# Kernel tuning notes

Hardware: AMD Instinct MI355X
Metric: run time of the kernel (lower is better)

The kernel has to match this reference:

```python
import jax, jax.numpy as jnp
import numpy as np

D = 768
H = 8
HD = D // H
FF = 4 * D


def _linear_params(key, din, dout):
    kw, kb = jax.random.split(key)
    lim = 1.0 / np.sqrt(din)
    W = jax.random.uniform(kw, (din, dout), jnp.float32, -lim, lim)
    b = jax.random.uniform(kb, (dout,), jnp.float32, -lim, lim)
    return W, b


def setup_inputs() -> dict:
    key = jax.random.key(0)
    ks = jax.random.split(key, 8)
    x = jax.random.normal(ks[0], (16, 1024, D), jnp.float32)
    Wq, bq = _linear_params(ks[1], D, D)
    Wk, bk = _linear_params(ks[2], D, D)
    Wv, bv = _linear_params(ks[3], D, D)
    Wo, bo = _linear_params(ks[4], D, D)
    W1, b1 = _linear_params(ks[5], D, FF)
    W2, b2 = _linear_params(ks[6], FF, D)
    gamma = jnp.ones((D,), jnp.float32)
    beta = jnp.zeros((D,), jnp.float32)
    return {"x": x, "gamma": gamma, "beta": beta,
            "Wq": Wq, "bq": bq, "Wk": Wk, "bk": bk, "Wv": Wv, "bv": bv,
            "Wo": Wo, "bo": bo, "W1": W1, "b1": b1, "W2": W2, "b2": b2}


def _layernorm(x, gamma, beta, eps=1e-5):
    mu = jnp.mean(x, axis=-1, keepdims=True)
    var = jnp.var(x, axis=-1, keepdims=True)
    return (x - mu) * jax.lax.rsqrt(var + eps) * gamma + beta


def _block(x, gamma, beta, Wq, bq, Wk, bk, Wv, bv, Wo, bo, W1, b1, W2, b2):
    b, n, d = x.shape
    residual = x
    h = _layernorm(x, gamma, beta)
    # QKV projections -> [b, h, n, hd]
    q = (h @ Wq + bq).reshape(b, n, H, HD).transpose(0, 2, 1, 3)
    k = (h @ Wk + bk).reshape(b, n, H, HD).transpose(0, 2, 1, 3)
    v = (h @ Wv + bv).reshape(b, n, H, HD).transpose(0, 2, 1, 3)
    scale = HD ** 0.5
    scores = jnp.einsum('bhid,bhjd->bhij', q, k) / scale
    attn = jax.nn.softmax(scores, axis=-1)
    out = jnp.einsum('bhij,bhjd->bhid', attn, v)
    out = out.transpose(0, 2, 1, 3).reshape(b, n, d)
    out = out @ Wo + bo
    out = out + residual
    residual = out
    h = _layernorm(out, gamma, beta)  # same LN params reused (as in source)
    h = jax.nn.gelu(h @ W1 + b1, approximate=False)
    h = h @ W2 + b2
    return h + residual


def reference(x, gamma, beta, Wq, bq, Wk, bk, Wv, bv, Wo, bo, W1, b1, W2, b2):
    return _block(x, gamma, beta, Wq, bq, Wk, bk, Wv, bv, Wo, bo, W1, b1, W2, b2)
```

## Files before the change

### kernel.cpp

```cpp
#include <hip/hip_runtime.h>

typedef unsigned short u16;
typedef float f32x4 __attribute__((ext_vector_type(4)));
typedef __bf16 bf16x8 __attribute__((ext_vector_type(8)));

#define AS1 __attribute__((address_space(1)))
#define AS3 __attribute__((address_space(3)))

__device__ __forceinline__ float bf2f(u16 h) {
  return __uint_as_float(((unsigned)h) << 16);
}
__device__ __forceinline__ u16 f2bf(float f) {
  unsigned u = __float_as_uint(f);
  unsigned r = (u + 0x7FFFu + ((u >> 16) & 1u)) >> 16;
  return (u16)r;
}
__device__ __forceinline__ void gload16(const u16* g, u16* l) {
  __builtin_amdgcn_global_load_lds((const AS1 void*)g, (AS3 void*)l, 16, 0, 0);
}

__global__ void transpose_k(const float* __restrict__ in, u16* __restrict__ out,
                            int R, int C) {
  __shared__ u16 t[32][33];
  int c0 = blockIdx.x * 32, r0 = blockIdx.y * 32;
  int tx = threadIdx.x & 31, ty = threadIdx.x >> 5;
  for (int i = 0; i < 32; i += 8)
    t[ty + i][tx] = f2bf(in[(size_t)(r0 + ty + i) * C + c0 + tx]);
  __syncthreads();
  for (int i = 0; i < 32; i += 8)
    out[(size_t)(c0 + ty + i) * R + r0 + tx] = t[tx][ty + i];
}

__global__ void vtrans_k(const u16* __restrict__ v, u16* __restrict__ vt) {
  __shared__ u16 t[32][33];
  int bh = blockIdx.z, b = bh >> 3, h = bh & 7;
  int n0 = blockIdx.y * 32, d0 = blockIdx.x * 32;
  int tx = threadIdx.x & 31, ty = threadIdx.x >> 5;
  const u16* src = v + (size_t)(b * 1024) * 768 + h * 96;
  for (int i = 0; i < 32; i += 8)
    t[ty + i][tx] = src[(size_t)(n0 + ty + i) * 768 + d0 + tx];
  __syncthreads();
  u16* dst = vt + ((size_t)bh * 96 + d0) * 1024 + n0;
  for (int i = 0; i < 32; i += 8)
    dst[(size_t)(ty + i) * 1024 + tx] = t[tx][ty + i];
}

__global__ __launch_bounds__(256) void ln_f32_k(const float* __restrict__ x,
                                                const float* __restrict__ gamma,
                                                const float* __restrict__ beta,
                                                u16* __restrict__ out) {
  __shared__ float red[8];
  int row = blockIdx.x, t = threadIdx.x;
  const float* xr = x + (size_t)row * 768;
  float v[3], s = 0.f, s2 = 0.f;
#pragma unroll
  for (int i = 0; i < 3; i++) {
    v[i] = xr[t + i * 256];
    s += v[i]; s2 += v[i] * v[i];
  }
#pragma unroll
  for (int off = 1; off < 64; off <<= 1) {
    s += __shfl_xor(s, off, 64);
    s2 += __shfl_xor(s2, off, 64);
  }
  int w = t >> 6;
  if ((t & 63) == 0) { red[w] = s; red[4 + w] = s2; }
  __syncthreads();
  s = red[0] + red[1] + red[2] + red[3];
  s2 = red[4] + red[5] + red[6] + red[7];
  float mu = s * (1.f / 768.f);
  float var = s2 * (1.f / 768.f) - mu * mu;
  float rs = rsqrtf(var + 1e-5f);
  u16* orow = out + (size_t)row * 768;
#pragma unroll
  for (int i = 0; i < 3; i++) {
    int c = t + i * 256;
    orow[c] = f2bf((v[i] - mu) * rs * gamma[c] + beta[c]);
  }
}

#define BM 128
#define BN 128
#define BK 64

template <int EPI>
__global__ __launch_bounds__(256, 2) void gemm_bt(
    const u16* __restrict__ A, const u16* __restrict__ Bt,
    const float* __restrict__ bias, const float* __restrict__ res,
    void* __restrict__ Cv, int M, int N, int K) {
  __shared__ u16 As[BM * BK];
  __shared__ u16 Bs[BN * BK];
  int tid = threadIdx.x, lane = tid & 63, w = tid >> 6;
  int l15 = lane & 15, quad = lane >> 4;
  int wm = (w >> 1) * 64, wn = (w & 1) * 64;
  int GX = gridDim.x;
  int f = blockIdx.y * GX + blockIdx.x;
  int mpx = GX >> 3;
  int xcd = f & 7, idx = f >> 3;
  int m0 = (xcd * mpx + (idx % mpx)) * BM;
  int n0 = (idx / mpx) * BN;
  int srow = lane >> 3;
  int scol = ((lane & 7) ^ srow) * 8;
  f32x4 acc[4][4] = {};
  for (int k0 = 0; k0 < K; k0 += BK) {
    __syncthreads();
#pragma unroll
    for (int i = 0; i < 4; i++) {
      int c = w * 4 + i;
      int r = c * 8 + srow;
      gload16(A + (size_t)(m0 + r) * K + k0 + scol, As + c * 512);
      gload16(Bt + (size_t)(n0 + r) * K + k0 + scol, Bs + c * 512);
    }
    __syncthreads();
#pragma unroll
    for (int kk = 0; kk < 2; kk++) {
      bf16x8 af[4], bfv[4];
      int sa = ((kk * 4 + quad) ^ (l15 & 7)) * 8;
#pragma unroll
      for (int i = 0; i < 4; i++) {
        af[i] = *(const bf16x8*)(As + (wm + i * 16 + l15) * BK + sa);
        bfv[i] = *(const bf16x8*)(Bs + (wn + i * 16 + l15) * BK + sa);
      }
#pragma unroll
      for (int mt = 0; mt < 4; mt++)
#pragma unroll
        for (int nt = 0; nt < 4; nt++)
          acc[mt][nt] = __builtin_amdgcn_mfma_f32_16x16x32_bf16(
              af[mt], bfv[nt], acc[mt][nt], 0, 0, 0);
    }
  }
#pragma unroll
  for (int nt = 0; nt < 4; nt++) {
    int col = n0 + wn + nt * 16 + l15;
    float bv = bias[col];
#pragma unroll
    for (int mt = 0; mt < 4; mt++) {
      int row = m0 + wm + mt * 16 + quad * 4;
#pragma unroll
      for (int r = 0; r < 4; r++) {
        float v = acc[mt][nt][r] + bv;
        size_t idx2 = (size_t)(row + r) * N + col;
        if (EPI == 4) {
          v += res[idx2];
          ((float*)Cv)[idx2] = v;
        } else {
          if (EPI == 2) v = 0.5f * v * (1.0f + erff(v * 0.70710678118654752f));
          ((u16*)Cv)[idx2] = f2bf(v);
        }
      }
    }
  }
}

#define QSS 104
#define VSS 72
#define PSS 72
__global__ __launch_bounds__(256, 2) void attn_k(const u16* __restrict__ q,
                                                 const u16* __restrict__ k,
                                                 const u16* __restrict__ vt,
                                                 u16* __restrict__ o) {
  __shared__ u16 qs[64 * QSS];
  __shared__ u16 ks[2][64 * QSS];
  __shared__ u16 vts[2][96 * VSS];
  __shared__ u16 ps[4 * 16 * PSS];
  int tid = threadIdx.x, lane = tid & 63, w = tid >> 6;
  int l15 = lane & 15, quad = lane >> 4;
  {
  }
  int f = blockIdx.y * 16 + blockIdx.x;
  int xcd = f & 7, idx = f >> 3;
  int bh = xcd * 16 + (idx & 15);
  int qt = idx >> 4;
  int b = bh >> 3, h = bh & 7;
  const u16* qbase = q + (size_t)(b * 1024 + qt * 64) * 768 + h * 96;
  const u16* kbase = k + (size_t)(b * 1024) * 768 + h * 96;
  const u16* vtbase = vt + (size_t)bh * 96 * 1024;
  int kr[3], ko[3], vr[3], vo[3];
#pragma unroll
  for (int i = 0; i < 3; i++) {
    int c = tid + i * 256;
    kr[i] = c / 12; ko[i] = (c % 12) * 8;
    vr[i] = c >> 3; vo[i] = (c & 7) * 8;
  }
#pragma unroll
  for (int i = 0; i < 3; i++)
    *(uint4*)(qs + kr[i] * QSS + ko[i]) =
        *(const uint4*)(qbase + (size_t)kr[i] * 768 + ko[i]);
  uint4 kreg[3], vreg[3];
#pragma unroll
  for (int i = 0; i < 3; i++) {
    kreg[i] = *(const uint4*)(kbase + (size_t)kr[i] * 768 + ko[i]);
    vreg[i] = *(const uint4*)(vtbase + (size_t)vr[i] * 1024 + vo[i]);
  }
#pragma unroll
  for (int i = 0; i < 3; i++) {
    *(uint4*)(ks[0] + kr[i] * QSS + ko[i]) = kreg[i];
    *(uint4*)(vts[0] + vr[i] * VSS + vo[i]) = vreg[i];
  }
  __syncthreads();

  float mi[4], li[4];
#pragma unroll
  for (int r = 0; r < 4; r++) { mi[r] = -1e30f; li[r] = 0.f; }
  f32x4 oacc[6] = {};
  const float scale = 0.10206207261596577f;
  for (int kt = 0; kt < 16; kt++) {
    int cur = kt & 1, nxt = cur ^ 1;
    int ktn = (kt + 1) & 15;
#pragma unroll
    for (int i = 0; i < 3; i++) {
      kreg[i] = *(const uint4*)(kbase + (size_t)(ktn * 64 + kr[i]) * 768 + ko[i]);
      vreg[i] = *(const uint4*)(vtbase + (size_t)vr[i] * 1024 + ktn * 64 + vo[i]);
    }
    f32x4 s[4] = {};
#pragma unroll
    for (int kk = 0; kk < 3; kk++) {
      bf16x8 a = *(const bf16x8*)(qs + (w * 16 + l15) * QSS + kk * 32 + quad * 8);
#pragma unroll
      for (int nt = 0; nt < 4; nt++) {
        bf16x8 bb =
            *(const bf16x8*)(ks[cur] + (nt * 16 + l15) * QSS + kk * 32 + quad * 8);
        s[nt] = __builtin_amdgcn_mfma_f32_16x16x32_bf16(a, bb, s[nt], 0, 0, 0);
      }
    }
#pragma unroll
    for (int r = 0; r < 4; r++) {
      float sv[4], mx = -1e30f;
#pragma unroll
      for (int nt = 0; nt < 4; nt++) {
        sv[nt] = s[nt][r];
        mx = fmaxf(mx, sv[nt]);
      }
#pragma unroll
      for (int off = 1; off < 16; off <<= 1) mx = fmaxf(mx, __shfl_xor(mx, off, 16));
      float mnew = fmaxf(mi[r], mx);
      float alpha = __expf((mi[r] - mnew) * scale);
      float rs = 0.f;
#pragma unroll
      for (int nt = 0; nt < 4; nt++) {
        sv[nt] = __expf((sv[nt] - mnew) * scale);
        rs += sv[nt];
      }
      li[r] = li[r] * alpha + rs;
      mi[r] = mnew;
#pragma unroll
      for (int ht = 0; ht < 6; ht++) oacc[ht][r] *= alpha;
      int prow = quad * 4 + r;
#pragma unroll
      for (int nt = 0; nt < 4; nt++)
        ps[w * 16 * PSS + prow * PSS + nt * 16 + l15] = f2bf(sv[nt]);
    }
    asm volatile("s_waitcnt lgkmcnt(0)" ::: "memory");
#pragma unroll
    for (int kk = 0; kk < 2; kk++) {
      bf16x8 a = *(const bf16x8*)(ps + w * 16 * PSS + l15 * PSS + kk * 32 + quad * 8);
#pragma unroll
      for (int ht = 0; ht < 6; ht++) {
        bf16x8 bb =
            *(const bf16x8*)(vts[cur] + (ht * 16 + l15) * VSS + kk * 32 + quad * 8);
        oacc[ht] = __builtin_amdgcn_mfma_f32_16x16x32_bf16(a, bb, oacc[ht], 0, 0, 0);
      }
    }
#pragma unroll
    for (int i = 0; i < 3; i++) {
      *(uint4*)(ks[nxt] + kr[i] * QSS + ko[i]) = kreg[i];
      *(uint4*)(vts[nxt] + vr[i] * VSS + vo[i]) = vreg[i];
    }
    __syncthreads();
  }
#pragma unroll
  for (int r = 0; r < 4; r++)
#pragma unroll
    for (int off = 1; off < 16; off <<= 1) li[r] += __shfl_xor(li[r], off, 16);
  u16* obase = o + (size_t)(b * 1024 + qt * 64 + w * 16) * 768 + h * 96;
#pragma unroll
  for (int r = 0; r < 4; r++) {
    float inv = 1.0f / li[r];
    int row = quad * 4 + r;
#pragma unroll
    for (int ht = 0; ht < 6; ht++)
      obase[(size_t)row * 768 + ht * 16 + l15] = f2bf(oacc[ht][r] * inv);
  }
}

extern "C" void kernel_launch(void* const* d_in, const int* in_sizes, int n_in,
                              void* d_out, int out_size, void* d_ws,
                              size_t ws_size, hipStream_t stream) {
  const float* x = (const float*)d_in[0];
  const float* gamma = (const float*)d_in[1];
  const float* beta = (const float*)d_in[2];
  const float* Wq = (const float*)d_in[3];
  const float* bq = (const float*)d_in[4];
  const float* Wk = (const float*)d_in[5];
  const float* bk = (const float*)d_in[6];
  const float* Wv = (const float*)d_in[7];
  const float* bv = (const float*)d_in[8];
  const float* Wo = (const float*)d_in[9];
  const float* bo = (const float*)d_in[10];
  const float* W1 = (const float*)d_in[11];
  const float* b1 = (const float*)d_in[12];
  const float* W2 = (const float*)d_in[13];
  const float* b2 = (const float*)d_in[14];
  float* out = (float*)d_out;

  char* ws = (char*)d_ws;
  size_t off = 0;
  auto alloc = [&](size_t elems) {
    u16* p = (u16*)(ws + off);
    off += elems * sizeof(u16);
    return p;
  };
  u16* WqT = alloc(768 * 768);
  u16* WkT = alloc(768 * 768);
  u16* WvT = alloc(768 * 768);
  u16* WoT = alloc(768 * 768);
  u16* W1T = alloc((size_t)768 * 3072);
  u16* W2T = alloc((size_t)3072 * 768);
  u16* hb = alloc((size_t)16384 * 768);
  u16* qb = alloc((size_t)16384 * 768);
  u16* kb = alloc((size_t)16384 * 768);
  u16* vb = alloc((size_t)16384 * 768);

  transpose_k<<<dim3(24, 24), 256, 0, stream>>>(Wq, WqT, 768, 768);
  transpose_k<<<dim3(24, 24), 256, 0, stream>>>(Wk, WkT, 768, 768);
  transpose_k<<<dim3(24, 24), 256, 0, stream>>>(Wv, WvT, 768, 768);
  transpose_k<<<dim3(24, 24), 256, 0, stream>>>(Wo, WoT, 768, 768);
  transpose_k<<<dim3(96, 24), 256, 0, stream>>>(W1, W1T, 768, 3072);
  transpose_k<<<dim3(24, 96), 256, 0, stream>>>(W2, W2T, 3072, 768);

  ln_f32_k<<<16384, 256, 0, stream>>>(x, gamma, beta, hb);
  gemm_bt<0><<<dim3(128, 6), 256, 0, stream>>>(hb, WqT, bq, nullptr, qb,
                                               16384, 768, 768);
  gemm_bt<0><<<dim3(128, 6), 256, 0, stream>>>(hb, WkT, bk, nullptr, kb,
                                               16384, 768, 768);
  gemm_bt<0><<<dim3(128, 6), 256, 0, stream>>>(hb, WvT, bv, nullptr, vb,
                                               16384, 768, 768);
  vtrans_k<<<dim3(3, 32, 128), 256, 0, stream>>>(vb, hb);
  attn_k<<<dim3(16, 128), 256, 0, stream>>>(qb, kb, hb, vb);
  gemm_bt<4><<<dim3(128, 6), 256, 0, stream>>>(vb, WoT, bo, x, out,
                                               16384, 768, 768);
  ln_f32_k<<<16384, 256, 0, stream>>>(out, gamma, beta, kb);
  for (int c = 0; c < 4; c++) {
    const u16* h2c = kb + (size_t)c * 4096 * 768;
    const float* y1c = out + (size_t)c * 4096 * 768;
    float* outc = out + (size_t)c * 4096 * 768;
    gemm_bt<2><<<dim3(32, 24), 256, 0, stream>>>(h2c, W1T, b1, nullptr, vb,
                                                 4096, 3072, 768);
    gemm_bt<4><<<dim3(32, 6), 256, 0, stream>>>(vb, W2T, b2, y1c, outc,
                                                4096, 768, 3072);
  }
}
```

Before: 820.7 us.

## Fuse QKV projections into one GEMM and double-buffer GEMM LDS tiles

Merges the three Q/K/V projection GEMMs into a single GEMM of width 2304. It does this by packing the biases and relying on the transposed Wq/Wk/Wv buffers sitting contiguously in the workspace, so the activation tile is loaded once instead of three times. The GEMM kernel now double-buffers its A/B shared-memory tiles with one barrier per K step, and stages each fragment so every lane reads it contiguously. Attention writes its output into the unused V slot of the packed QKV buffer, and the output projection reads it through a new leading-dimension parameter. The FFN is processed in two larger chunks instead of four. The cost is twice the LDS per block and a dependence on the workspace allocation order.

```diff
diff --git a/kernel.cpp b/kernel.cpp
--- a/kernel.cpp
+++ b/kernel.cpp
@@ -31,14 +31,21 @@
     out[(size_t)(c0 + ty + i) * R + r0 + tx] = t[tx][ty + i];
 }
 
-__global__ void vtrans_k(const u16* __restrict__ v, u16* __restrict__ vt) {
+__global__ void pack3_k(const float* __restrict__ a, const float* __restrict__ b,
+                        const float* __restrict__ c, float* __restrict__ out) {
+  int i = blockIdx.x * 256 + threadIdx.x;
+  float v = (i < 768) ? a[i] : (i < 1536) ? b[i - 768] : c[i - 1536];
+  out[i] = v;
+}
+
+__global__ void vtrans_k(const u16* __restrict__ qkv, u16* __restrict__ vt) {
   __shared__ u16 t[32][33];
   int bh = blockIdx.z, b = bh >> 3, h = bh & 7;
   int n0 = blockIdx.y * 32, d0 = blockIdx.x * 32;
   int tx = threadIdx.x & 31, ty = threadIdx.x >> 5;
-  const u16* src = v + (size_t)(b * 1024) * 768 + h * 96;
+  const u16* src = qkv + (size_t)(b * 1024) * 2304 + 1536 + h * 96;
   for (int i = 0; i < 32; i += 8)
-    t[ty + i][tx] = src[(size_t)(n0 + ty + i) * 768 + d0 + tx];
+    t[ty + i][tx] = src[(size_t)(n0 + ty + i) * 2304 + d0 + tx];
   __syncthreads();
   u16* dst = vt + ((size_t)bh * 96 + d0) * 1024 + n0;
   for (int i = 0; i < 32; i += 8)
@@ -87,9 +94,9 @@
 __global__ __launch_bounds__(256, 2) void gemm_bt(
     const u16* __restrict__ A, const u16* __restrict__ Bt,
     const float* __restrict__ bias, const float* __restrict__ res,
-    void* __restrict__ Cv, int M, int N, int K) {
-  __shared__ u16 As[BM * BK];
-  __shared__ u16 Bs[BN * BK];
+    void* __restrict__ Cv, int M, int N, int K, int lda) {
+  __shared__ u16 As[2][BM * BK];
+  __shared__ u16 Bs[2][BN * BK];
   int tid = threadIdx.x, lane = tid & 63, w = tid >> 6;
   int l15 = lane & 15, quad = lane >> 4;
   int wm = (w >> 1) * 64, wn = (w & 1) * 64;
@@ -99,27 +106,44 @@
   int xcd = f & 7, idx = f >> 3;
   int m0 = (xcd * mpx + (idx % mpx)) * BM;
   int n0 = (idx / mpx) * BN;
-  int srow = lane >> 3;
-  int scol = ((lane & 7) ^ srow) * 8;
+  int sr[4], sc[4];
+#pragma unroll
+  for (int i = 0; i < 4; i++) {
+    int c = w * 4 + i;
+    sr[i] = (c >> 1) * 16 + l15;
+    sc[i] = (c & 1) * 32 + quad * 8;
+  }
+  int NT = K / BK;
+#pragma unroll
+  for (int i = 0; i < 4; i++) {
+    int c = w * 4 + i;
+    gload16(A + (size_t)(m0 + sr[i]) * lda + sc[i], As[0] + c * 512);
+    gload16(Bt + (size_t)(n0 + sr[i]) * K + sc[i], Bs[0] + c * 512);
+  }
+  __syncthreads();
   f32x4 acc[4][4] = {};
-  for (int k0 = 0; k0 < K; k0 += BK) {
-    __syncthreads();
-#pragma unroll
-    for (int i = 0; i < 4; i++) {
-      int c = w * 4 + i;
-      int r = c * 8 + srow;
-      gload16(A + (size_t)(m0 + r) * K + k0 + scol, As + c * 512);
-      gload16(Bt + (size_t)(n0 + r) * K + k0 + scol, Bs + c * 512);
-    }
-    __syncthreads();
+  for (int t = 0; t < NT; t++) {
+    int cur = t & 1;
+    if (t + 1 < NT) {
+      int k0 = (t + 1) * BK;
+#pragma unroll
+      for (int i = 0; i < 4; i++) {
+        int c = w * 4 + i;
+        gload16(A + (size_t)(m0 + sr[i]) * lda + k0 + sc[i], As[cur ^ 1] + c * 512);
+        gload16(Bt + (size_t)(n0 + sr[i]) * K + k0 + sc[i], Bs[cur ^ 1] + c * 512);
+      }
+    }
+    const u16* ab = As[cur];
+    const u16* bb = Bs[cur];
 #pragma unroll
     for (int kk = 0; kk < 2; kk++) {
       bf16x8 af[4], bfv[4];
-      int sa = ((kk * 4 + quad) ^ (l15 & 7)) * 8;
 #pragma unroll
       for (int i = 0; i < 4; i++) {
-        af[i] = *(const bf16x8*)(As + (wm + i * 16 + l15) * BK + sa);
-        bfv[i] = *(const bf16x8*)(Bs + (wn + i * 16 + l15) * BK + sa);
+        int i2a = (w >> 1) * 4 + i;
+        int i2b = (w & 1) * 4 + i;
+        af[i] = *(const bf16x8*)(ab + (i2a * 2 + kk) * 512 + lane * 8);
+        bfv[i] = *(const bf16x8*)(bb + (i2b * 2 + kk) * 512 + lane * 8);
       }
 #pragma unroll
       for (int mt = 0; mt < 4; mt++)
@@ -128,6 +152,7 @@
           acc[mt][nt] = __builtin_amdgcn_mfma_f32_16x16x32_bf16(
               af[mt], bfv[nt], acc[mt][nt], 0, 0, 0);
     }
+    __syncthreads();
   }
 #pragma unroll
   for (int nt = 0; nt < 4; nt++) {
@@ -155,25 +180,22 @@
 #define QSS 104
 #define VSS 72
 #define PSS 72
-__global__ __launch_bounds__(256, 2) void attn_k(const u16* __restrict__ q,
-                                                 const u16* __restrict__ k,
-                                                 const u16* __restrict__ vt,
-                                                 u16* __restrict__ o) {
+#define QST 2304
+__global__ __launch_bounds__(256, 2) void attn_k(u16* __restrict__ qkv,
+                                                 const u16* __restrict__ vt) {
   __shared__ u16 qs[64 * QSS];
   __shared__ u16 ks[2][64 * QSS];
   __shared__ u16 vts[2][96 * VSS];
   __shared__ u16 ps[4 * 16 * PSS];
   int tid = threadIdx.x, lane = tid & 63, w = tid >> 6;
   int l15 = lane & 15, quad = lane >> 4;
-  {
-  }
   int f = blockIdx.y * 16 + blockIdx.x;
   int xcd = f & 7, idx = f >> 3;
   int bh = xcd * 16 + (idx & 15);
   int qt = idx >> 4;
   int b = bh >> 3, h = bh & 7;
-  const u16* qbase = q + (size_t)(b * 1024 + qt * 64) * 768 + h * 96;
-  const u16* kbase = k + (size_t)(b * 1024) * 768 + h * 96;
+  const u16* qbase = qkv + (size_t)(b * 1024 + qt * 64) * QST + h * 96;
+  const u16* kbase = qkv + (size_t)(b * 1024) * QST + 768 + h * 96;
   const u16* vtbase = vt + (size_t)bh * 96 * 1024;
   int kr[3], ko[3], vr[3], vo[3];
 #pragma unroll
@@ -185,11 +207,11 @@
 #pragma unroll
   for (int i = 0; i < 3; i++)
     *(uint4*)(qs + kr[i] * QSS + ko[i]) =
-        *(const uint4*)(qbase + (size_t)kr[i] * 768 + ko[i]);
+        *(const uint4*)(qbase + (size_t)kr[i] * QST + ko[i]);
   uint4 kreg[3], vreg[3];
 #pragma unroll
   for (int i = 0; i < 3; i++) {
-    kreg[i] = *(const uint4*)(kbase + (size_t)kr[i] * 768 + ko[i]);
+    kreg[i] = *(const uint4*)(kbase + (size_t)kr[i] * QST + ko[i]);
     vreg[i] = *(const uint4*)(vtbase + (size_t)vr[i] * 1024 + vo[i]);
   }
 #pragma unroll
@@ -209,7 +231,7 @@
     int ktn = (kt + 1) & 15;
 #pragma unroll
     for (int i = 0; i < 3; i++) {
-      kreg[i] = *(const uint4*)(kbase + (size_t)(ktn * 64 + kr[i]) * 768 + ko[i]);
+      kreg[i] = *(const uint4*)(kbase + (size_t)(ktn * 64 + kr[i]) * QST + ko[i]);
       vreg[i] = *(const uint4*)(vtbase + (size_t)vr[i] * 1024 + ktn * 64 + vo[i]);
     }
     f32x4 s[4] = {};
@@ -272,14 +294,14 @@
   for (int r = 0; r < 4; r++)
 #pragma unroll
     for (int off = 1; off < 16; off <<= 1) li[r] += __shfl_xor(li[r], off, 16);
-  u16* obase = o + (size_t)(b * 1024 + qt * 64 + w * 16) * 768 + h * 96;
+  u16* obase = qkv + (size_t)(b * 1024 + qt * 64 + w * 16) * QST + 1536 + h * 96;
 #pragma unroll
   for (int r = 0; r < 4; r++) {
     float inv = 1.0f / li[r];
     int row = quad * 4 + r;
 #pragma unroll
     for (int ht = 0; ht < 6; ht++)
-      obase[(size_t)row * 768 + ht * 16 + l15] = f2bf(oacc[ht][r] * inv);
+      obase[(size_t)row * QST + ht * 16 + l15] = f2bf(oacc[ht][r] * inv);
   }
 }
 
@@ -316,10 +338,9 @@
   u16* WoT = alloc(768 * 768);
   u16* W1T = alloc((size_t)768 * 3072);
   u16* W2T = alloc((size_t)3072 * 768);
-  u16* hb = alloc((size_t)16384 * 768);
-  u16* qb = alloc((size_t)16384 * 768);
-  u16* kb = alloc((size_t)16384 * 768);
-  u16* vb = alloc((size_t)16384 * 768);
+  float* bqkv = (float*)(ws + off); off += 2304 * sizeof(float);
+  u16* buf1 = alloc((size_t)16384 * 768);
+  u16* buf2 = alloc((size_t)16384 * 2304);
 
   transpose_k<<<dim3(24, 24), 256, 0, stream>>>(Wq, WqT, 768, 768);
   transpose_k<<<dim3(24, 24), 256, 0, stream>>>(Wk, WkT, 768, 768);
@@ -327,26 +348,23 @@
   transpose_k<<<dim3(24, 24), 256, 0, stream>>>(Wo, WoT, 768, 768);
   transpose_k<<<dim3(96, 24), 256, 0, stream>>>(W1, W1T, 768, 3072);
   transpose_k<<<dim3(24, 96), 256, 0, stream>>>(W2, W2T, 3072, 768);
-
-  ln_f32_k<<<16384, 256, 0, stream>>>(x, gamma, beta, hb);
-  gemm_bt<0><<<dim3(128, 6), 256, 0, stream>>>(hb, WqT, bq, nullptr, qb,
-                                               16384, 768, 768);
-  gemm_bt<0><<<dim3(128, 6), 256, 0, stream>>>(hb, WkT, bk, nullptr, kb,
-                                               16384, 768, 768);
-  gemm_bt<0><<<dim3(128, 6), 256, 0, stream>>>(hb, WvT, bv, nullptr, vb,
-                                               16384, 768, 768);
-  vtrans_k<<<dim3(3, 32, 128), 256, 0, stream>>>(vb, hb);
-  attn_k<<<dim3(16, 128), 256, 0, stream>>>(qb, kb, hb, vb);
-  gemm_bt<4><<<dim3(128, 6), 256, 0, stream>>>(vb, WoT, bo, x, out,
-                                               16384, 768, 768);
-  ln_f32_k<<<16384, 256, 0, stream>>>(out, gamma, beta, kb);
-  for (int c = 0; c < 4; c++) {
-    const u16* h2c = kb + (size_t)c * 4096 * 768;
-    const float* y1c = out + (size_t)c * 4096 * 768;
-    float* outc = out + (size_t)c * 4096 * 768;
-    gemm_bt<2><<<dim3(32, 24), 256, 0, stream>>>(h2c, W1T, b1, nullptr, vb,
-                                                 4096, 3072, 768);
-    gemm_bt<4><<<dim3(32, 6), 256, 0, stream>>>(vb, W2T, b2, y1c, outc,
-                                                4096, 768, 3072);
-  }
-}
+  pack3_k<<<9, 256, 0, stream>>>(bq, bk, bv, bqkv);
+
+  ln_f32_k<<<16384, 256, 0, stream>>>(x, gamma, beta, buf1);
+  gemm_bt<0><<<dim3(128, 18), 256, 0, stream>>>(buf1, WqT, bqkv, nullptr,
+                                                buf2, 16384, 2304, 768, 768);
+  vtrans_k<<<dim3(3, 32, 128), 256, 0, stream>>>(buf2, buf1);
+  attn_k<<<dim3(16, 128), 256, 0, stream>>>(buf2, buf1);
+  gemm_bt<4><<<dim3(128, 6), 256, 0, stream>>>(buf2 + 1536, WoT, bo, x, out,
+                                               16384, 768, 768, 2304);
+  ln_f32_k<<<16384, 256, 0, stream>>>(out, gamma, beta, buf1);
+  for (int c = 0; c < 2; c++) {
+    const u16* h2c = buf1 + (size_t)c * 8192 * 768;
+    const float* y1c = out + (size_t)c * 8192 * 768;
+    float* outc = out + (size_t)c * 8192 * 768;
+    gemm_bt<2><<<dim3(64, 24), 256, 0, stream>>>(h2c, W1T, b1, nullptr, buf2,
+                                                 8192, 3072, 768, 768);
+    gemm_bt<4><<<dim3(64, 6), 256, 0, stream>>>(buf2, W2T, b2, y1c, outc,
+                                                8192, 768, 3072, 3072);
+  }
+}
```

Result: slower. 901.1 us (+9.8%).

## Double-buffer GEMM LDS tiles with prefetch and fragment-ordered layout; enlarge FFN chunks

Applied to the files above, without the earlier changes.

The bf16 GEMM now holds two LDS buffers for A and B, so global_load_lds of the next K tile is issued while MFMAs run on the current tile, with one barrier per iteration instead of two. The LDS tile layout changes from an XOR-swizzled row-major layout to chunks ordered by MFMA fragment, so each lane reads 16 contiguous bytes and the address arithmetic is simpler. A separate lda parameter is added, and the FFN is processed in two 8192-row chunks instead of four, using hb as the GELU intermediate. The trade-offs are doubled LDS per block and a larger intermediate buffer. That buffer spills past hb into the adjacent qb allocation, which is only safe if the allocations are contiguous.

```diff
diff --git a/kernel.cpp b/kernel.cpp
--- a/kernel.cpp
+++ b/kernel.cpp
@@ -87,9 +87,9 @@
 __global__ __launch_bounds__(256, 2) void gemm_bt(
     const u16* __restrict__ A, const u16* __restrict__ Bt,
     const float* __restrict__ bias, const float* __restrict__ res,
-    void* __restrict__ Cv, int M, int N, int K) {
-  __shared__ u16 As[BM * BK];
-  __shared__ u16 Bs[BN * BK];
+    void* __restrict__ Cv, int M, int N, int K, int lda) {
+  __shared__ u16 As[2][BM * BK];
+  __shared__ u16 Bs[2][BN * BK];
   int tid = threadIdx.x, lane = tid & 63, w = tid >> 6;
   int l15 = lane & 15, quad = lane >> 4;
   int wm = (w >> 1) * 64, wn = (w & 1) * 64;
@@ -99,27 +99,44 @@
   int xcd = f & 7, idx = f >> 3;
   int m0 = (xcd * mpx + (idx % mpx)) * BM;
   int n0 = (idx / mpx) * BN;
-  int srow = lane >> 3;
-  int scol = ((lane & 7) ^ srow) * 8;
+  int sr[4], sc[4];
+#pragma unroll
+  for (int i = 0; i < 4; i++) {
+    int c = w * 4 + i;
+    sr[i] = (c >> 1) * 16 + l15;
+    sc[i] = (c & 1) * 32 + quad * 8;
+  }
+  int NT = K / BK;
+#pragma unroll
+  for (int i = 0; i < 4; i++) {
+    int c = w * 4 + i;
+    gload16(A + (size_t)(m0 + sr[i]) * lda + sc[i], As[0] + c * 512);
+    gload16(Bt + (size_t)(n0 + sr[i]) * K + sc[i], Bs[0] + c * 512);
+  }
+  __syncthreads();
   f32x4 acc[4][4] = {};
-  for (int k0 = 0; k0 < K; k0 += BK) {
-    __syncthreads();
-#pragma unroll
-    for (int i = 0; i < 4; i++) {
-      int c = w * 4 + i;
-      int r = c * 8 + srow;
-      gload16(A + (size_t)(m0 + r) * K + k0 + scol, As + c * 512);
-      gload16(Bt + (size_t)(n0 + r) * K + k0 + scol, Bs + c * 512);
-    }
-    __syncthreads();
+  for (int t = 0; t < NT; t++) {
+    int cur = t & 1;
+    if (t + 1 < NT) {
+      int k0 = (t + 1) * BK;
+#pragma unroll
+      for (int i = 0; i < 4; i++) {
+        int c = w * 4 + i;
+        gload16(A + (size_t)(m0 + sr[i]) * lda + k0 + sc[i], As[cur ^ 1] + c * 512);
+        gload16(Bt + (size_t)(n0 + sr[i]) * K + k0 + sc[i], Bs[cur ^ 1] + c * 512);
+      }
+    }
+    const u16* ab = As[cur];
+    const u16* bb = Bs[cur];
 #pragma unroll
     for (int kk = 0; kk < 2; kk++) {
       bf16x8 af[4], bfv[4];
-      int sa = ((kk * 4 + quad) ^ (l15 & 7)) * 8;
 #pragma unroll
       for (int i = 0; i < 4; i++) {
-        af[i] = *(const bf16x8*)(As + (wm + i * 16 + l15) * BK + sa);
-        bfv[i] = *(const bf16x8*)(Bs + (wn + i * 16 + l15) * BK + sa);
+        int i2a = (w >> 1) * 4 + i;
+        int i2b = (w & 1) * 4 + i;
+        af[i] = *(const bf16x8*)(ab + (i2a * 2 + kk) * 512 + lane * 8);
+        bfv[i] = *(const bf16x8*)(bb + (i2b * 2 + kk) * 512 + lane * 8);
       }
 #pragma unroll
       for (int mt = 0; mt < 4; mt++)
@@ -128,6 +145,7 @@
           acc[mt][nt] = __builtin_amdgcn_mfma_f32_16x16x32_bf16(
               af[mt], bfv[nt], acc[mt][nt], 0, 0, 0);
     }
+    __syncthreads();
   }
 #pragma unroll
   for (int nt = 0; nt < 4; nt++) {
@@ -165,8 +183,6 @@
   __shared__ u16 ps[4 * 16 * PSS];
   int tid = threadIdx.x, lane = tid & 63, w = tid >> 6;
   int l15 = lane & 15, quad = lane >> 4;
-  {
-  }
   int f = blockIdx.y * 16 + blockIdx.x;
   int xcd = f & 7, idx = f >> 3;
   int bh = xcd * 16 + (idx & 15);
@@ -330,23 +346,24 @@
 
   ln_f32_k<<<16384, 256, 0, stream>>>(x, gamma, beta, hb);
   gemm_bt<0><<<dim3(128, 6), 256, 0, stream>>>(hb, WqT, bq, nullptr, qb,
-                                               16384, 768, 768);
+                                               16384, 768, 768, 768);
   gemm_bt<0><<<dim3(128, 6), 256, 0, stream>>>(hb, WkT, bk, nullptr, kb,
-                                               16384, 768, 768);
+                                               16384, 768, 768, 768);
   gemm_bt<0><<<dim3(128, 6), 256, 0, stream>>>(hb, WvT, bv, nullptr, vb,
-                                               16384, 768, 768);
+                                               16384, 768, 768, 768);
   vtrans_k<<<dim3(3, 32, 128), 256, 0, stream>>>(vb, hb);
   attn_k<<<dim3(16, 128), 256, 0, stream>>>(qb, kb, hb, vb);
   gemm_bt<4><<<dim3(128, 6), 256, 0, stream>>>(vb, WoT, bo, x, out,
-                                               16384, 768, 768);
+                                               16384, 768, 768, 768);
   ln_f32_k<<<16384, 256, 0, stream>>>(out, gamma, beta, kb);
-  for (int c = 0; c < 4; c++) {
-    const u16* h2c = kb + (size_t)c * 4096 * 768;
-    const float* y1c = out + (size_t)c * 4096 * 768;
-    float* outc = out + (size_t)c * 4096 * 768;
-    gemm_bt<2><<<dim3(32, 24), 256, 0, stream>>>(h2c, W1T, b1, nullptr, vb,
-                                                 4096, 3072, 768);
-    gemm_bt<4><<<dim3(32, 6), 256, 0, stream>>>(vb, W2T, b2, y1c, outc,
-                                                4096, 768, 3072);
-  }
-}
+  u16* fbuf = hb;
+  for (int c = 0; c < 2; c++) {
+    const u16* h2c = kb + (size_t)c * 8192 * 768;
+    const float* y1c = out + (size_t)c * 8192 * 768;
+    float* outc = out + (size_t)c * 8192 * 768;
+    gemm_bt<2><<<dim3(64, 24), 256, 0, stream>>>(h2c, W1T, b1, nullptr, fbuf,
+                                                 8192, 3072, 768, 768);
+    gemm_bt<4><<<dim3(64, 6), 256, 0, stream>>>(fbuf, W2T, b2, y1c, outc,
+                                                8192, 768, 3072, 3072);
+  }
+}
```

Measured after the change: 886.2 us. 1.08x slower.
